# Performance work log

Hardware: AMD Instinct MI355X
Metric: run time of the kernel (lower is better)

The kernel has to match this reference:

```python
import jax, jax.numpy as jnp
import numpy as np

B, S, D, L = 8, 512, 768, 200


def leaky(x, slope=0.2):
    return jnp.where(x >= 0, x, slope * x)


def l1_normalize(x, axis):
    # torch.nn.functional.normalize(p=1): x / max(sum|x|, 1e-12)
    return x / jnp.maximum(jnp.sum(jnp.abs(x), axis=axis, keepdims=True), 1e-12)


def setup_inputs() -> dict:
    key = jax.random.key(0)
    ks = jax.random.split(key, 16)
    s = 1.0 / np.sqrt(D)
    return {
        "doc_embedding": jax.random.normal(ks[0], (B, S, D), jnp.float32),
        "labels": jax.random.uniform(ks[1], (B, L), jnp.float32),
        "label_embed": jax.random.normal(ks[2], (L, D), jnp.float32),
        "label_adj": jax.random.uniform(ks[3], (L, L), jnp.float32),
        "w_gcn3": jax.random.uniform(ks[4], (D, D), jnp.float32, -s, s),
        "w_gcn5": jax.random.uniform(ks[5], (D, D), jnp.float32, -s, s),
        "w_ll1": jax.random.normal(ks[6], (D, D), jnp.float32) * s,
        "b_ll1": jax.random.normal(ks[7], (D,), jnp.float32) * s,
        "w_ll2": jax.random.normal(ks[8], (D, D), jnp.float32) * s,
        "b_ll2": jax.random.normal(ks[9], (D,), jnp.float32) * s,
        "w_lin": jax.random.normal(ks[10], (2 * D, D), jnp.float32) * (1.0 / np.sqrt(2 * D)),
        "b_lin": jax.random.normal(ks[11], (D,), jnp.float32) * s,
        "conv_w": jax.random.normal(ks[12], (L, 1, 9, 9), jnp.float32) * (1.0 / 9.0),
        "conv_b": jax.random.normal(ks[13], (L,), jnp.float32) * 0.01,
        "w_lin1": jax.random.normal(ks[14], (D, L), jnp.float32) * s,
        "b_lin1": jax.random.normal(ks[15], (L,), jnp.float32) * s,
    }


def reference(doc_embedding, labels, label_embed, label_adj, w_gcn3, w_gcn5,
              w_ll1, b_ll1, w_ll2, b_ll2, w_lin, b_lin, conv_w, conv_b,
              w_lin1, b_lin1):
    b = doc_embedding.shape[0]
    # stacked (replicated) label embeddings: [B, L, D]
    le = jnp.broadcast_to(label_embed, (b,) + label_embed.shape)

    # GCN3: adj @ (x @ W), leaky relu 0.2
    le = leaky(jnp.einsum('lm,bmd->bld', label_adj, le @ w_gcn3))

    # learned adjacency A = sigmoid(lin1(le) @ lin2(le)^T)   [B, L, L]
    q = le @ w_ll1 + b_ll1
    k = le @ w_ll2 + b_ll2
    A = jax.nn.sigmoid(jnp.einsum('bld,bmd->blm', q, k))

    # normalize_adj: D^{-1/2} with detached row sum; out = (A D)^T D
    row_sum = jax.lax.stop_gradient(jnp.sum(A, axis=1))  # [B, L]
    d_inv_sqrt = jnp.where(row_sum > 0, row_sum ** -0.5, 0.0)
    AD = A * d_inv_sqrt[:, None, :]                 # A @ diag(d)
    A_norm = jnp.swapaxes(AD, 1, 2) * d_inv_sqrt[:, None, :]

    # GCN5 with learned adj
    d_le = leaky(jnp.einsum('blm,bmd->bld', A_norm, le @ w_gcn5))

    le_cat = jnp.concatenate([le, d_le], axis=-1)   # [B, L, 2D]
    le_out = le_cat @ w_lin + b_lin                 # [B, L, D]

    le_out = l1_normalize(le_out, axis=-2)
    doc = l1_normalize(doc_embedding, axis=-2)

    # word-label attention map [B, S, L]
    wla = jnp.einsum('bsd,bld->bsl', doc, le_out)

    # conv2d 1 -> L channels, 9x9, pad 4 over [B, 1, S, L]
    att = jax.lax.conv_general_dilated(
        wla[:, None, :, :], conv_w, window_strides=(1, 1),
        padding=((4, 4), (4, 4)),
        dimension_numbers=('NCHW', 'OIHW', 'NCHW'))
    att = att + conv_b[None, :, None, None]         # [B, L, S, L]

    att = jnp.max(att, axis=1)                      # [B, S, L]
    att = jnp.max(att, axis=-1, keepdims=True)      # [B, S, 1]
    gate = jnp.tanh(att)

    h_enc = jnp.sum(gate * doc, axis=1)             # [B, D]
    label_output = jax.nn.sigmoid(h_enc @ w_lin1 + b_lin1)

    eps = 1e-7
    p = jnp.clip(label_output, eps, 1.0 - eps)
    loss = -jnp.mean(labels * jnp.log(p) + (1.0 - labels) * jnp.log(1.0 - p))
    return label_output, loss
```

## Files before the change

kernel.cpp:

```cpp
#include <hip/hip_runtime.h>
#include <hip/hip_bf16.h>
#include <math.h>

#define BB 8
#define SS 512
#define DD 768
#define LL 200

typedef __attribute__((ext_vector_type(8))) short bf16x8;
typedef __attribute__((ext_vector_type(4))) float f32x4;

__device__ inline short f2bf(float f) {
    unsigned u = __builtin_bit_cast(unsigned, f);
    unsigned r = (u + 0x7FFFu + ((u >> 16) & 1u)) >> 16;
    return (short)r;
}

#define LDP2 72

template<int EPI, bool TB>
__global__ __launch_bounds__(256) void mgemm_k(
    const short* __restrict__ A, int lda,
    const void* __restrict__ Bv, int ldb,
    const float* __restrict__ bias,
    const void* __restrict__ Bv2, const float* __restrict__ bias2, int nsplit,
    const void* __restrict__ Bv3, const float* __restrict__ bias3, int nsplit2,
    float* __restrict__ Cf, int ldc,
    short* __restrict__ Cb, int ldcb,
    short* __restrict__ Ct, int ldct, int nsplitT,
    int M, int N, int K)
{
    __shared__ __align__(16) short As[64 * LDP2];
    __shared__ __align__(16) short Bs[64 * LDP2];
    const int tid = threadIdx.x;
    const int bm = blockIdx.y * 64;
    const int bn = blockIdx.x * 64;
    int bnb = bn;
    if (!TB) {
        if (bn >= nsplit2)      { Bv = Bv3; bias = bias3; bnb = bn - nsplit2; }
        else if (bn >= nsplit)  { Bv = Bv2; bias = bias2; bnb = bn - nsplit; }
    }
    const int w = tid >> 6, lane = tid & 63, g = lane >> 4, ln = lane & 15;
    const int Kp = (K + 63) & ~63;
    const int nt = Kp >> 6;

    const int ar = tid >> 2, ac = tid & 3;
    const int bkk = tid >> 2, bc = tid & 3;

    f32x4 acc[4];
    #pragma unroll
    for (int i = 0; i < 4; ++i) acc[i] = (f32x4){0.f, 0.f, 0.f, 0.f};

    bf16x8 aR0 = {0,0,0,0,0,0,0,0}, aR1 = {0,0,0,0,0,0,0,0};
    bf16x8 bR0 = {0,0,0,0,0,0,0,0}, bR1 = {0,0,0,0,0,0,0,0};
    float  bF[16];
    #pragma unroll
    for (int j = 0; j < 16; ++j) bF[j] = 0.f;

    const int gmS = bm + ar;
    const bool aOk = (gmS < M);

    auto fetchA = [&](int k0) {
        if (aOk) {
            const short* p = A + (size_t)gmS * lda + k0 + ac * 16;
            aR0 = *(const bf16x8*)p;
            aR1 = *(const bf16x8*)(p + 8);
        }
    };
    auto fetchB = [&](int k0) {
        if (TB) {
            const short* Bt = (const short*)Bv;
            int gn = bn + ar;
            if (gn < N) {
                const short* p = Bt + (size_t)gn * ldb + k0 + ac * 16;
                bR0 = *(const bf16x8*)p;
                bR1 = *(const bf16x8*)(p + 8);
            }
        } else {
            const float* Bp = (const float*)Bv;
            int gk = k0 + bkk;
            int n0 = bnb + bc * 16;
            int gn0 = bn + bc * 16;
            if (gk < K) {
                const float* p = Bp + (size_t)gk * ldb + n0;
                if (gn0 + 16 <= N) {
                    #pragma unroll
                    for (int q = 0; q < 4; ++q) {
                        float4 x = *(const float4*)(p + q * 4);
                        bF[q*4+0]=x.x; bF[q*4+1]=x.y; bF[q*4+2]=x.z; bF[q*4+3]=x.w;
                    }
                } else {
                    #pragma unroll
                    for (int j = 0; j < 16; ++j) bF[j] = (gn0 + j < N) ? p[j] : 0.f;
                }
            } else {
                #pragma unroll
                for (int j = 0; j < 16; ++j) bF[j] = 0.f;
            }
        }
    };

    fetchA(0);
    fetchB(0);

    for (int t = 0; t < nt; ++t) {
        {
            short* pa = As + ar * LDP2 + ac * 16;
            *(bf16x8*)pa = aR0;
            *(bf16x8*)(pa + 8) = aR1;
        }
        if (TB) {
            short* pb = Bs + ar * LDP2 + ac * 16;
            *(bf16x8*)pb = bR0;
            *(bf16x8*)(pb + 8) = bR1;
        } else {
            #pragma unroll
            for (int j = 0; j < 16; ++j)
                Bs[(bc * 16 + j) * LDP2 + bkk] = f2bf(bF[j]);
        }
        __syncthreads();

        if (t + 1 < nt) {
            int k0 = (t + 1) << 6;
            fetchA(k0);
            fetchB(k0);
        }

        #pragma unroll
        for (int ks = 0; ks < 2; ++ks) {
            bf16x8 a = *(const bf16x8*)(As + (w * 16 + ln) * LDP2 + ks * 32 + g * 8);
            #pragma unroll
            for (int nb = 0; nb < 4; ++nb) {
                bf16x8 b = *(const bf16x8*)(Bs + (nb * 16 + ln) * LDP2 + ks * 32 + g * 8);
                acc[nb] = __builtin_amdgcn_mfma_f32_16x16x32_bf16(a, b, acc[nb], 0, 0, 0);
            }
        }
        __syncthreads();
    }

    #pragma unroll
    for (int nb = 0; nb < 4; ++nb) {
        int gn = bn + nb * 16 + ln;
        float bv = (bias && gn < N) ? bias[bnb + nb * 16 + ln] : 0.f;
        #pragma unroll
        for (int r = 0; r < 4; ++r) {
            int gm = bm + w * 16 + g * 4 + r;
            if (gm < M && gn < N) {
                float v = acc[nb][r] + bv;
                if (EPI == 1) v = (v >= 0.f) ? v : 0.2f * v;
                else if (EPI == 2) v = 1.f / (1.f + expf(-v));
                if (Cf) Cf[(size_t)gm * ldc + gn] = v;
                if (Cb) Cb[(size_t)gm * ldcb + gn] = f2bf(v);
                if (Ct && gn >= nsplitT)
                    Ct[(size_t)(gn - nsplitT) * ldct + gm] = f2bf(v);
            }
        }
    }
}

#define WP 168
#define TP 24
#define WTR 217
#define WROWS 208
#define APAD 256
#define BIGN (1 << 30)

__global__ void prep_k(const float* __restrict__ cw, const float* __restrict__ cb,
                       const float* __restrict__ adj,
                       short* __restrict__ wkg, short* __restrict__ adj_bf)
{
    int idx = blockIdx.x * blockDim.x + threadIdx.x;
    if (idx < WROWS * WP) {
        int o = idx / WP, kk = idx % WP;
        int kj = kk >> 4, ki = kk & 15;
        float v = 0.f;
        if (o < LL && kj < 9) {
            if (ki < 9) v = cw[o * 81 + ki * 9 + kj];
            else if (ki == 9 && kj == 0) v = cb[o];
        }
        wkg[idx] = f2bf(v);
        return;
    }
    idx -= WROWS * WP;
    if (idx < LL * APAD) {
        int r = idx / APAD, c = idx % APAD;
        adj_bf[idx] = f2bf(c < LL ? adj[r * LL + c] : 0.f);
    }
}

__global__ void ca_k(const float* __restrict__ A, short* __restrict__ An)
{
    int i = blockIdx.x;
    int j = threadIdx.x;
    float si = 0.f, sj = 0.f;
    for (int l = 0; l < LL; ++l) {
        si += A[l * LL + i];
        if (j < LL) sj += A[l * LL + j];
    }
    float di = (si > 0.f) ? (1.f / sqrtf(si)) : 0.f;
    float dj = (sj > 0.f) ? (1.f / sqrtf(sj)) : 0.f;
    float v = (j < LL) ? A[j * LL + i] * di * dj : 0.f;
    An[i * APAD + j] = f2bf(v);
}

__global__ void l1n_k(const float* __restrict__ X, short* __restrict__ Xb)
{
    int c = threadIdx.x >> 5, r = threadIdx.x & 31;
    int col = blockIdx.x * 8 + c;
    float s = 0.f;
    for (int l = r; l < LL; l += 32) s += fabsf(X[l * DD + col]);
    #pragma unroll
    for (int off = 16; off > 0; off >>= 1) s += __shfl_xor(s, off, 64);
    float inv = 1.f / fmaxf(s, 1e-12f);
    for (int l = r; l < LL; l += 32)
        Xb[l * DD + col] = f2bf(X[l * DD + col] * inv);
}

__global__ void docsum_k(const float* __restrict__ doc, float* __restrict__ denom)
{
    int dc = blockIdx.x, b = blockIdx.y;
    int dx = threadIdx.x & 63, sy = threadIdx.x >> 6;
    int d = dc * 64 + dx;
    float s = 0.f;
    for (int t = sy; t < SS; t += 4)
        s += fabsf(doc[((size_t)b * SS + t) * DD + d]);
    __shared__ float red[4][64];
    red[sy][dx] = s;
    __syncthreads();
    if (sy == 0)
        denom[b * DD + d] = fmaxf(red[0][dx] + red[1][dx] + red[2][dx] + red[3][dx], 1e-12f);
}

__global__ void docbf_k(const float* __restrict__ doc, const float* __restrict__ denom,
                        short* __restrict__ docb)
{
    int gid = blockIdx.x * blockDim.x + threadIdx.x;
    if (gid >= BB * SS * DD / 4) return;
    size_t base = (size_t)gid * 4;
    int d = (int)(base % DD);
    int b = (int)(base / ((size_t)SS * DD));
    float4 v = *(const float4*)(doc + base);
    float4 dn = *(const float4*)(denom + b * DD + d);
    short4 o;
    o.x = f2bf(v.x / dn.x);
    o.y = f2bf(v.y / dn.y);
    o.z = f2bf(v.z / dn.z);
    o.w = f2bf(v.w / dn.w);
    *(short4*)(docb + base) = o;
}

__global__ __launch_bounds__(512, 1) void conv_max_k(
    const float* __restrict__ wla,
    const short* __restrict__ wkg,
    float* __restrict__ gate)
{
    extern __shared__ short smem[];
    short* Wk   = smem;
    short* winT = Wk + WROWS * WP;
    short* wbf  = winT + 4 * WTR * TP;
    __shared__ float wredf[8];

    const int blk = blockIdx.x;
    const int b = blk >> 7;
    const int s0 = (blk & 127) << 2;
    const int tid = threadIdx.x;

    {
        const int4* src = (const int4*)wkg;
        int4* dst = (int4*)Wk;
        for (int i = tid; i < WROWS * WP / 8; i += 512) dst[i] = src[i];
    }
    for (int idx = tid; idx < 12 * 216; idx += 512) {
        int r = idx / 216, c = idx % 216;
        int sr = s0 - 4 + r, col = c - 4;
        float v = 0.f;
        if (sr >= 0 && sr < SS && col >= 0 && col < LL)
            v = wla[((size_t)b * SS + sr) * LL + col];
        wbf[idx] = f2bf(v);
    }
    __syncthreads();
    for (int idx = tid; idx < 4 * WTR; idx += 512) {
        int p = idx / WTR, r = idx % WTR;
        short vals[16];
        #pragma unroll
        for (int i = 0; i < 9; ++i) vals[i] = (r < 216) ? wbf[(p + i) * 216 + r] : (short)0;
        vals[9] = (short)0x3F80;
        #pragma unroll
        for (int i = 10; i < 16; ++i) vals[i] = 0;
        short* dstp = winT + (p * WTR + r) * TP;
        *(bf16x8*)dstp = *(const bf16x8*)vals;
        *(bf16x8*)(dstp + 8) = *(const bf16x8*)(vals + 8);
    }
    __syncthreads();

    const int w = tid >> 6;
    const int p = w >> 1;
    const int h = w & 1;
    const int lane = tid & 63;
    const int g = lane >> 4;
    const int ln = lane & 15;
    const short* WT = winT + p * WTR * TP;

    bf16x8 Af[7][5];
    #pragma unroll
    for (int s = 0; s < 7; ++s) {
        int st = h * 7 + s;
        if (st > 12) st = 12;
        #pragma unroll
        for (int j = 0; j < 5; ++j)
            Af[s][j] = *(const bf16x8*)(Wk + (st * 16 + ln) * WP + j * 32 + g * 8);
    }

    float lm = -INFINITY;

    auto loadB = [&](int nt, bf16x8 (&Bf)[5]) {
        #pragma unroll
        for (int j = 0; j < 5; ++j)
            Bf[j] = *(const bf16x8*)(WT + (nt * 16 + ln + 2 * j + (g >> 1)) * TP + (g & 1) * 8);
    };
    auto compute = [&](int nt, const bf16x8 (&Bf)[5]) {
        #pragma unroll
        for (int s = 0; s < 7; ++s) {
            if (h == 0 || s < 6) {
                int st = h * 7 + s;
                f32x4 acc = {0.f, 0.f, 0.f, 0.f};
                #pragma unroll
                for (int j = 0; j < 5; ++j)
                    acc = __builtin_amdgcn_mfma_f32_16x16x32_bf16(Af[s][j], Bf[j], acc, 0, 0, 0);
                float t = fmaxf(fmaxf(acc[0], acc[1]), fmaxf(acc[2], acc[3]));
                bool ok = (st < 12 || g < 2) && (nt < 12 || ln < 8);
                lm = ok ? fmaxf(lm, t) : lm;
            }
        }
    };

    bf16x8 B0[5], B1[5];
    loadB(0, B0);
    for (int nt = 0; nt < 12; nt += 2) {
        loadB(nt + 1, B1);
        compute(nt, B0);
        loadB(nt + 2, B0);
        compute(nt + 1, B1);
    }
    compute(12, B0);

    #pragma unroll
    for (int off = 32; off > 0; off >>= 1)
        lm = fmaxf(lm, __shfl_xor(lm, off, 64));
    if (lane == 0) wredf[w] = lm;
    __syncthreads();
    if (tid < 4)
        gate[((size_t)b << 9) + s0 + tid] = tanhf(fmaxf(wredf[2 * tid], wredf[2 * tid + 1]));
}

__global__ void henc_part_k(const float* __restrict__ doc, const float* __restrict__ gate,
                            float* __restrict__ hpart)
{
    int dc = blockIdx.x, sc = blockIdx.y, b = blockIdx.z;
    int dx = threadIdx.x & 63, sy = threadIdx.x >> 6;
    int d = dc * 64 + dx;
    float s = 0.f;
    for (int t = sy; t < 64; t += 4) {
        int srow = sc * 64 + t;
        s = fmaf(doc[((size_t)b * SS + srow) * DD + d], gate[b * SS + srow], s);
    }
    __shared__ float red[4][64];
    red[sy][dx] = s;
    __syncthreads();
    if (sy == 0)
        hpart[((size_t)b * 8 + sc) * DD + d] = red[0][dx] + red[1][dx] + red[2][dx] + red[3][dx];
}

__global__ void final2_k(const float* __restrict__ hpart, const float* __restrict__ denom,
                         const float* __restrict__ W, const float* __restrict__ bias,
                         float* __restrict__ out)
{
    int b = blockIdx.x, tid = threadIdx.x;
    __shared__ float hb[DD];
    for (int idx = tid; idx < DD; idx += 256) {
        float s = 0.f;
        #pragma unroll
        for (int sc = 0; sc < 8; ++sc) s += hpart[((size_t)b * 8 + sc) * DD + idx];
        hb[idx] = s / denom[b * DD + idx];
    }
    __syncthreads();
    int l = tid;
    if (l < LL) {
        float acc = bias[l];
        for (int d = 0; d < DD; ++d) acc = fmaf(hb[d], W[d * LL + l], acc);
        out[b * LL + l] = 1.f / (1.f + expf(-acc));
    }
}

__global__ void loss_k(const float* __restrict__ out, const float* __restrict__ labels,
                       float* __restrict__ loss_out)
{
    float s = 0.f;
    for (int i = threadIdx.x; i < BB * LL; i += 256) {
        float p = out[i];
        p = fminf(fmaxf(p, 1e-7f), 1.f - 1e-7f);
        float y = labels[i];
        s += y * logf(p) + (1.f - y) * logf(1.f - p);
    }
    #pragma unroll
    for (int off = 32; off > 0; off >>= 1) s += __shfl_down(s, off, 64);
    __shared__ float ws[4];
    if ((threadIdx.x & 63) == 0) ws[threadIdx.x >> 6] = s;
    __syncthreads();
    if (threadIdx.x == 0)
        loss_out[0] = -(ws[0] + ws[1] + ws[2] + ws[3]) / (float)(BB * LL);
}

static void mgemm(hipStream_t st, int epi, bool tb,
                  const short* A, int lda, const void* B, int ldb,
                  const float* bias,
                  const void* B2, const float* bias2, int nsplit,
                  const void* B3, const float* bias3, int nsplit2,
                  float* Cf, int ldc, short* Cb, int ldcb,
                  short* Ct, int ldct, int nsplitT,
                  int M, int N, int K)
{
    dim3 g((N + 63) / 64, (M + 63) / 64);
    if (!tb) {
        if (epi == 0)      mgemm_k<0, false><<<g, 256, 0, st>>>(A, lda, B, ldb, bias, B2, bias2, nsplit, B3, bias3, nsplit2, Cf, ldc, Cb, ldcb, Ct, ldct, nsplitT, M, N, K);
        else if (epi == 1) mgemm_k<1, false><<<g, 256, 0, st>>>(A, lda, B, ldb, bias, B2, bias2, nsplit, B3, bias3, nsplit2, Cf, ldc, Cb, ldcb, Ct, ldct, nsplitT, M, N, K);
        else               mgemm_k<2, false><<<g, 256, 0, st>>>(A, lda, B, ldb, bias, B2, bias2, nsplit, B3, bias3, nsplit2, Cf, ldc, Cb, ldcb, Ct, ldct, nsplitT, M, N, K);
    } else {
        if (epi == 0)      mgemm_k<0, true><<<g, 256, 0, st>>>(A, lda, B, ldb, bias, B2, bias2, nsplit, B3, bias3, nsplit2, Cf, ldc, Cb, ldcb, Ct, ldct, nsplitT, M, N, K);
        else if (epi == 1) mgemm_k<1, true><<<g, 256, 0, st>>>(A, lda, B, ldb, bias, B2, bias2, nsplit, B3, bias3, nsplit2, Cf, ldc, Cb, ldcb, Ct, ldct, nsplitT, M, N, K);
        else               mgemm_k<2, true><<<g, 256, 0, st>>>(A, lda, B, ldb, bias, B2, bias2, nsplit, B3, bias3, nsplit2, Cf, ldc, Cb, ldcb, Ct, ldct, nsplitT, M, N, K);
    }
}

extern "C" void kernel_launch(void* const* d_in, const int* in_sizes, int n_in,
                              void* d_out, int out_size, void* d_ws, size_t ws_size,
                              hipStream_t stream)
{
    const float* doc_emb   = (const float*)d_in[0];
    const float* labels    = (const float*)d_in[1];
    const float* label_emb = (const float*)d_in[2];
    const float* label_adj = (const float*)d_in[3];
    const float* w_gcn3    = (const float*)d_in[4];
    const float* w_gcn5    = (const float*)d_in[5];
    const float* w_ll1     = (const float*)d_in[6];
    const float* b_ll1     = (const float*)d_in[7];
    const float* w_ll2     = (const float*)d_in[8];
    const float* b_ll2     = (const float*)d_in[9];
    const float* w_lin     = (const float*)d_in[10];
    const float* b_lin     = (const float*)d_in[11];
    const float* conv_w    = (const float*)d_in[12];
    const float* conv_b    = (const float*)d_in[13];
    const float* w_lin1    = (const float*)d_in[14];
    const float* b_lin1    = (const float*)d_in[15];

    float* out = (float*)d_out;

    char* p = (char*)d_ws;
    auto alloc = [&](size_t bytes) { void* r = p; p += (bytes + 15) & ~(size_t)15; return r; };
    short* wkg       = (short*)alloc(WROWS * WP * 2);
    short* adj_bf    = (short*)alloc(200 * APAD * 2);
    short* E2_bf     = (short*)alloc(200 * 768 * 2);
    short* le_cat_bf = (short*)alloc(200 * 1536 * 2);
    short* qkh_bf    = (short*)alloc(200 * 2304 * 2);
    short* Ht        = (short*)alloc(768 * 256 * 2);
    float* Amat      = (float*)alloc(200 * 200 * 4);
    short* Anorm_bf  = (short*)alloc(200 * APAD * 2);
    float* le_out_f  = (float*)alloc(200 * 768 * 4);
    short* le_out_bf = (short*)alloc(200 * 768 * 2);
    float* denom     = (float*)alloc(BB * DD * 4);
    short* doc_nb    = (short*)alloc((size_t)BB * SS * DD * 2);
    float* wla       = (float*)alloc((size_t)BB * SS * LL * 4);
    float* gatev     = (float*)alloc(BB * SS * 4);
    float* hpart     = (float*)alloc(BB * 8 * DD * 4);

    prep_k<<<(WROWS * WP + LL * APAD + 255) / 256, 256, 0, stream>>>(
        conv_w, conv_b, label_adj, wkg, adj_bf);
    mgemm(stream, 0, false, adj_bf, APAD, label_emb, DD, nullptr,
          nullptr, nullptr, BIGN, nullptr, nullptr, BIGN,
          nullptr, 0, E2_bf, DD, nullptr, 0, BIGN, LL, DD, LL);
    mgemm(stream, 1, false, E2_bf, DD, w_gcn3, DD, nullptr,
          nullptr, nullptr, BIGN, nullptr, nullptr, BIGN,
          nullptr, 0, le_cat_bf, 1536, nullptr, 0, BIGN, LL, DD, DD);
    mgemm(stream, 0, false, le_cat_bf, 1536, w_ll1, DD, b_ll1,
          w_ll2, b_ll2, DD, w_gcn5, nullptr, 2 * DD,
          nullptr, 0, qkh_bf, 2304, Ht, 256, 2 * DD, LL, 3 * DD, DD);
    mgemm(stream, 2, true, qkh_bf, 2304, qkh_bf + DD, 2304, nullptr,
          nullptr, nullptr, BIGN, nullptr, nullptr, BIGN,
          Amat, LL, nullptr, 0, nullptr, 0, BIGN, LL, LL, DD);
    ca_k<<<LL, 256, 0, stream>>>(Amat, Anorm_bf);
    mgemm(stream, 1, true, Anorm_bf, APAD, Ht, 256, nullptr,
          nullptr, nullptr, BIGN, nullptr, nullptr, BIGN,
          nullptr, 0, le_cat_bf + DD, 1536, nullptr, 0, BIGN, LL, DD, LL);
    mgemm(stream, 0, false, le_cat_bf, 1536, w_lin, DD, b_lin,
          nullptr, nullptr, BIGN, nullptr, nullptr, BIGN,
          le_out_f, DD, nullptr, 0, nullptr, 0, BIGN, LL, DD, 2 * DD);
    l1n_k<<<96, 256, 0, stream>>>(le_out_f, le_out_bf);
    docsum_k<<<dim3(12, 8), 256, 0, stream>>>(doc_emb, denom);
    docbf_k<<<(BB * SS * DD / 4 + 255) / 256, 256, 0, stream>>>(doc_emb, denom, doc_nb);
    mgemm(stream, 0, true, doc_nb, DD, le_out_bf, DD, nullptr,
          nullptr, nullptr, BIGN, nullptr, nullptr, BIGN,
          wla, LL, nullptr, 0, nullptr, 0, BIGN, BB * SS, LL, DD);
    (void)hipFuncSetAttribute((const void*)conv_max_k,
                              hipFuncAttributeMaxDynamicSharedMemorySize, 116736);
    conv_max_k<<<1024, 512, 116736, stream>>>(wla, wkg, gatev);
    henc_part_k<<<dim3(12, 8, 8), 256, 0, stream>>>(doc_emb, gatev, hpart);
    final2_k<<<BB, 256, 0, stream>>>(hpart, denom, w_lin1, b_lin1, out);
    loss_k<<<1, 256, 0, stream>>>(out, labels, out + BB * LL);
}
```

Before: 298.3 us.

## Fuse doc normalization, store wla and reuse doc as bf16, restructure conv MFMA loop

Merges the doc column-sum and bf16 normalize kernels into one docnorm kernel, so the separate denom buffer and a launch go away. The wla GEMM now writes bf16 directly, conv reads bf16, and henc reads the normalized bf16 doc instead of fp32 doc plus a later divide. This roughly halves the traffic of the large intermediates. The conv inner loop is rewritten as a templated body that splits work per half, interleaves independent MFMA accumulators and drops the double-buffered B loads. The fused docnorm kernel uses only 96 blocks with strided column access, which may underuse bandwidth, and the bf16 doc in h_enc adds a small precision loss.

New measurement: 305.5 us. 2.4% more time.

```diff
diff --git a/kernel.cpp b/kernel.cpp
--- a/kernel.cpp
+++ b/kernel.cpp
@@ -14,6 +14,10 @@
     unsigned u = __builtin_bit_cast(unsigned, f);
     unsigned r = (u + 0x7FFFu + ((u >> 16) & 1u)) >> 16;
     return (short)r;
+}
+__device__ inline float bf2f(short s) {
+    unsigned u = ((unsigned)(unsigned short)s) << 16;
+    return __builtin_bit_cast(float, u);
 }
 
 #define LDP2 72
@@ -216,41 +220,64 @@
         Xb[l * DD + col] = f2bf(X[l * DD + col] * inv);
 }
 
-__global__ void docsum_k(const float* __restrict__ doc, float* __restrict__ denom)
+__global__ void docnorm_k(const float* __restrict__ doc, short* __restrict__ docb)
 {
     int dc = blockIdx.x, b = blockIdx.y;
     int dx = threadIdx.x & 63, sy = threadIdx.x >> 6;
     int d = dc * 64 + dx;
+    const float* pp = doc + (size_t)b * SS * DD + d;
     float s = 0.f;
-    for (int t = sy; t < SS; t += 4)
-        s += fabsf(doc[((size_t)b * SS + t) * DD + d]);
+    for (int t = sy; t < SS; t += 4) s += fabsf(pp[(size_t)t * DD]);
     __shared__ float red[4][64];
     red[sy][dx] = s;
     __syncthreads();
-    if (sy == 0)
-        denom[b * DD + d] = fmaxf(red[0][dx] + red[1][dx] + red[2][dx] + red[3][dx], 1e-12f);
-}
-
-__global__ void docbf_k(const float* __restrict__ doc, const float* __restrict__ denom,
-                        short* __restrict__ docb)
-{
-    int gid = blockIdx.x * blockDim.x + threadIdx.x;
-    if (gid >= BB * SS * DD / 4) return;
-    size_t base = (size_t)gid * 4;
-    int d = (int)(base % DD);
-    int b = (int)(base / ((size_t)SS * DD));
-    float4 v = *(const float4*)(doc + base);
-    float4 dn = *(const float4*)(denom + b * DD + d);
-    short4 o;
-    o.x = f2bf(v.x / dn.x);
-    o.y = f2bf(v.y / dn.y);
-    o.z = f2bf(v.z / dn.z);
-    o.w = f2bf(v.w / dn.w);
-    *(short4*)(docb + base) = o;
+    float dn = fmaxf(red[0][dx] + red[1][dx] + red[2][dx] + red[3][dx], 1e-12f);
+    float inv = 1.f / dn;
+    short* qq = docb + (size_t)b * SS * DD + d;
+    for (int t = sy; t < SS; t += 4) qq[(size_t)t * DD] = f2bf(pp[(size_t)t * DD] * inv);
+}
+
+template<int NS, int SOFF>
+__device__ __forceinline__ void conv_body(const short* __restrict__ Wk,
+                                          const short* __restrict__ WT,
+                                          int ln, int g, float& lm)
+{
+    bf16x8 Af[NS][5];
+    #pragma unroll
+    for (int s = 0; s < NS; ++s)
+        #pragma unroll
+        for (int j = 0; j < 5; ++j)
+            Af[s][j] = *(const bf16x8*)(Wk + ((SOFF + s) * 16 + ln) * WP + j * 32 + g * 8);
+
+    #pragma unroll 1
+    for (int nt = 0; nt < 13; ++nt) {
+        bf16x8 Bf[5];
+        #pragma unroll
+        for (int j = 0; j < 5; ++j)
+            Bf[j] = *(const bf16x8*)(WT + (nt * 16 + ln + 2 * j + (g >> 1)) * TP + (g & 1) * 8);
+
+        f32x4 acc[NS];
+        #pragma unroll
+        for (int s = 0; s < NS; ++s) acc[s] = (f32x4){0.f, 0.f, 0.f, 0.f};
+
+        #pragma unroll
+        for (int j = 0; j < 5; ++j)
+            #pragma unroll
+            for (int s = 0; s < NS; ++s)
+                acc[s] = __builtin_amdgcn_mfma_f32_16x16x32_bf16(Af[s][j], Bf[j], acc[s], 0, 0, 0);
+
+        bool colOK = (nt < 12) | (ln < 8);
+        #pragma unroll
+        for (int s = 0; s < NS; ++s) {
+            float t = fmaxf(fmaxf(acc[s][0], acc[s][1]), fmaxf(acc[s][2], acc[s][3]));
+            bool ok = colOK & ((SOFF + s < 12) | (g < 2));
+            lm = ok ? fmaxf(lm, t) : lm;
+        }
+    }
 }
 
 __global__ __launch_bounds__(512, 1) void conv_max_k(
-    const float* __restrict__ wla,
+    const short* __restrict__ wlab,
     const short* __restrict__ wkg,
     float* __restrict__ gate)
 {
@@ -273,10 +300,10 @@
     for (int idx = tid; idx < 12 * 216; idx += 512) {
         int r = idx / 216, c = idx % 216;
         int sr = s0 - 4 + r, col = c - 4;
-        float v = 0.f;
+        short v = 0;
         if (sr >= 0 && sr < SS && col >= 0 && col < LL)
-            v = wla[((size_t)b * SS + sr) * LL + col];
-        wbf[idx] = f2bf(v);
+            v = wlab[((size_t)b * SS + sr) * LL + col];
+        wbf[idx] = v;
     }
     __syncthreads();
     for (int idx = tid; idx < 4 * WTR; idx += 512) {
@@ -301,48 +328,9 @@
     const int ln = lane & 15;
     const short* WT = winT + p * WTR * TP;
 
-    bf16x8 Af[7][5];
-    #pragma unroll
-    for (int s = 0; s < 7; ++s) {
-        int st = h * 7 + s;
-        if (st > 12) st = 12;
-        #pragma unroll
-        for (int j = 0; j < 5; ++j)
-            Af[s][j] = *(const bf16x8*)(Wk + (st * 16 + ln) * WP + j * 32 + g * 8);
-    }
-
     float lm = -INFINITY;
-
-    auto loadB = [&](int nt, bf16x8 (&Bf)[5]) {
-        #pragma unroll
-        for (int j = 0; j < 5; ++j)
-            Bf[j] = *(const bf16x8*)(WT + (nt * 16 + ln + 2 * j + (g >> 1)) * TP + (g & 1) * 8);
-    };
-    auto compute = [&](int nt, const bf16x8 (&Bf)[5]) {
-        #pragma unroll
-        for (int s = 0; s < 7; ++s) {
-            if (h == 0 || s < 6) {
-                int st = h * 7 + s;
-                f32x4 acc = {0.f, 0.f, 0.f, 0.f};
-                #pragma unroll
-                for (int j = 0; j < 5; ++j)
-                    acc = __builtin_amdgcn_mfma_f32_16x16x32_bf16(Af[s][j], Bf[j], acc, 0, 0, 0);
-                float t = fmaxf(fmaxf(acc[0], acc[1]), fmaxf(acc[2], acc[3]));
-                bool ok = (st < 12 || g < 2) && (nt < 12 || ln < 8);
-                lm = ok ? fmaxf(lm, t) : lm;
-            }
-        }
-    };
-
-    bf16x8 B0[5], B1[5];
-    loadB(0, B0);
-    for (int nt = 0; nt < 12; nt += 2) {
-        loadB(nt + 1, B1);
-        compute(nt, B0);
-        loadB(nt + 2, B0);
-        compute(nt + 1, B1);
-    }
-    compute(12, B0);
+    if (h == 0) conv_body<7, 0>(Wk, WT, ln, g, lm);
+    else        conv_body<6, 7>(Wk, WT, ln, g, lm);
 
     #pragma unroll
     for (int off = 32; off > 0; off >>= 1)
@@ -353,7 +341,7 @@
         gate[((size_t)b << 9) + s0 + tid] = tanhf(fmaxf(wredf[2 * tid], wredf[2 * tid + 1]));
 }
 
-__global__ void henc_part_k(const float* __restrict__ doc, const float* __restrict__ gate,
+__global__ void henc_part_k(const short* __restrict__ doc_nb, const float* __restrict__ gate,
                             float* __restrict__ hpart)
 {
     int dc = blockIdx.x, sc = blockIdx.y, b = blockIdx.z;
@@ -362,7 +350,7 @@
     float s = 0.f;
     for (int t = sy; t < 64; t += 4) {
         int srow = sc * 64 + t;
-        s = fmaf(doc[((size_t)b * SS + srow) * DD + d], gate[b * SS + srow], s);
+        s = fmaf(bf2f(doc_nb[((size_t)b * SS + srow) * DD + d]), gate[b * SS + srow], s);
     }
     __shared__ float red[4][64];
     red[sy][dx] = s;
@@ -371,7 +359,7 @@
         hpart[((size_t)b * 8 + sc) * DD + d] = red[0][dx] + red[1][dx] + red[2][dx] + red[3][dx];
 }
 
-__global__ void final2_k(const float* __restrict__ hpart, const float* __restrict__ denom,
+__global__ void final2_k(const float* __restrict__ hpart,
                          const float* __restrict__ W, const float* __restrict__ bias,
                          float* __restrict__ out)
 {
@@ -381,7 +369,7 @@
         float s = 0.f;
         #pragma unroll
         for (int sc = 0; sc < 8; ++sc) s += hpart[((size_t)b * 8 + sc) * DD + idx];
-        hb[idx] = s / denom[b * DD + idx];
+        hb[idx] = s;
     }
     __syncthreads();
     int l = tid;
@@ -467,9 +455,8 @@
     short* Anorm_bf  = (short*)alloc(200 * APAD * 2);
     float* le_out_f  = (float*)alloc(200 * 768 * 4);
     short* le_out_bf = (short*)alloc(200 * 768 * 2);
-    float* denom     = (float*)alloc(BB * DD * 4);
     short* doc_nb    = (short*)alloc((size_t)BB * SS * DD * 2);
-    float* wla       = (float*)alloc((size_t)BB * SS * LL * 4);
+    short* wlab      = (short*)alloc((size_t)BB * SS * LL * 2);
     float* gatev     = (float*)alloc(BB * SS * 4);
     float* hpart     = (float*)alloc(BB * 8 * DD * 4);
 
@@ -495,15 +482,14 @@
           nullptr, nullptr, BIGN, nullptr, nullptr, BIGN,
           le_out_f, DD, nullptr, 0, nullptr, 0, BIGN, LL, DD, 2 * DD);
     l1n_k<<<96, 256, 0, stream>>>(le_out_f, le_out_bf);
-    docsum_k<<<dim3(12, 8), 256, 0, stream>>>(doc_emb, denom);
-    docbf_k<<<(BB * SS * DD / 4 + 255) / 256, 256, 0, stream>>>(doc_emb, denom, doc_nb);
+    docnorm_k<<<dim3(12, 8), 256, 0, stream>>>(doc_emb, doc_nb);
     mgemm(stream, 0, true, doc_nb, DD, le_out_bf, DD, nullptr,
           nullptr, nullptr, BIGN, nullptr, nullptr, BIGN,
-          wla, LL, nullptr, 0, nullptr, 0, BIGN, BB * SS, LL, DD);
+          nullptr, 0, wlab, LL, nullptr, 0, BIGN, BB * SS, LL, DD);
     (void)hipFuncSetAttribute((const void*)conv_max_k,
                               hipFuncAttributeMaxDynamicSharedMemorySize, 116736);
-    conv_max_k<<<1024, 512, 116736, stream>>>(wla, wkg, gatev);
-    henc_part_k<<<dim3(12, 8, 8), 256, 0, stream>>>(doc_emb, gatev, hpart);
-    final2_k<<<BB, 256, 0, stream>>>(hpart, denom, w_lin1, b_lin1, out);
+    conv_max_k<<<1024, 512, 116736, stream>>>(wlab, wkg, gatev);
+    henc_part_k<<<dim3(12, 8, 8), 256, 0, stream>>>(doc_nb, gatev, hpart);
+    final2_k<<<BB, 256, 0, stream>>>(hpart, w_lin1, b_lin1, out);
     loss_k<<<1, 256, 0, stream>>>(out, labels, out + BB * LL);
 }
```
